# Optimization experiments

Measured on AMD Instinct MI355X. Metric: run time of the kernel, lower is better.

Reference implementation:

```python
import jax, jax.numpy as jnp
import numpy as np

B, C, F, T = 4, 128, 64, 2048
QK_OUT = 4      # conv out channels for q/k
ATT_DIM = 10    # hard-coded linear out dim


def setup_inputs() -> dict:
    key = jax.random.key(0)
    ks = jax.random.split(key, 12)
    s = 0.05
    x = jax.random.normal(ks[0], (B, C, F, T), dtype=jnp.float32)
    Wq_conv = jax.random.normal(ks[1], (QK_OUT, C), dtype=jnp.float32) * s
    bq_conv = jax.random.normal(ks[2], (QK_OUT,), dtype=jnp.float32) * s
    Wq_lin = jax.random.normal(ks[3], (ATT_DIM, QK_OUT * F), dtype=jnp.float32) * s
    bq_lin = jax.random.normal(ks[4], (ATT_DIM,), dtype=jnp.float32) * s
    Wk_conv = jax.random.normal(ks[5], (QK_OUT, C), dtype=jnp.float32) * s
    bk_conv = jax.random.normal(ks[6], (QK_OUT,), dtype=jnp.float32) * s
    Wk_lin = jax.random.normal(ks[7], (ATT_DIM, QK_OUT * F), dtype=jnp.float32) * s
    bk_lin = jax.random.normal(ks[8], (ATT_DIM,), dtype=jnp.float32) * s
    Wv_conv = jax.random.normal(ks[9], (C, C), dtype=jnp.float32) * s
    bv_conv = jax.random.normal(ks[10], (C,), dtype=jnp.float32) * s
    return {
        "x": x,
        "Wq_conv": Wq_conv, "bq_conv": bq_conv,
        "Wq_lin": Wq_lin, "bq_lin": bq_lin,
        "Wk_conv": Wk_conv, "bk_conv": bk_conv,
        "Wk_lin": Wk_lin, "bk_lin": bk_lin,
        "Wv_conv": Wv_conv, "bv_conv": bv_conv,
    }


def reference(x, Wq_conv, bq_conv, Wq_lin, bq_lin,
              Wk_conv, bk_conv, Wk_lin, bk_lin, Wv_conv, bv_conv):
    b, c, f, t = x.shape
    # 1x1 conv == per-pixel channel matmul
    q = jnp.einsum('bcft,oc->boft', x, Wq_conv) + bq_conv[None, :, None, None]
    q = q.reshape(b, QK_OUT * f, t).transpose(0, 2, 1)          # [b, t, 4f]
    q = q @ Wq_lin.T + bq_lin                                    # [b, t, 10]
    k = jnp.einsum('bcft,oc->boft', x, Wk_conv) + bk_conv[None, :, None, None]
    k = k.reshape(b, QK_OUT * f, t).transpose(0, 2, 1)
    k = k @ Wk_lin.T + bk_lin                                    # [b, t, 10]
    energy = jnp.einsum('bid,bjd->bij', q, k)                    # [b, t, t]
    attention = jax.nn.softmax(energy, axis=-1)
    v = jnp.einsum('bcft,oc->boft', x, Wv_conv) + bv_conv[None, :, None, None]
    v = v.reshape(b, c * f, t)                                   # [b, cf, t]
    # out = value @ attention^T : out[n, i] = sum_j v[n, j] * attention[i, j]
    out = jnp.einsum('bnj,bij->bni', v, attention)
    return out.reshape(b, c, f, t)
```

## Files before the change

### kernel.cpp

```cpp
#include <hip/hip_runtime.h>
#include <hip/hip_bf16.h>

#define Bq 4
#define Cc 128
#define Ff 64
#define Tt 2048
#define CF 8192
#define NCHUNK 32
#define CHUNK 256

typedef __attribute__((ext_vector_type(4))) float f32x4;
typedef __attribute__((ext_vector_type(8))) short bf16x8;

__device__ inline ushort f2bf(float f) {
    __hip_bfloat16 h = __float2bfloat16(f);
    return *reinterpret_cast<ushort*>(&h);
}

__device__ inline void gload_lds16(const void* g, void* l) {
    __builtin_amdgcn_global_load_lds(
        (const __attribute__((address_space(1))) void*)g,
        (__attribute__((address_space(3))) void*)l, 16, 0, 0);
}

__global__ void k_prep(const float* __restrict__ Wq_lin, const float* __restrict__ Wq_conv,
                       const float* __restrict__ Wk_lin, const float* __restrict__ Wk_conv,
                       const float* __restrict__ bq_conv, const float* __restrict__ bq_lin,
                       const float* __restrict__ bk_conv, const float* __restrict__ bk_lin,
                       const float* __restrict__ Wv,
                       float* __restrict__ weff, float* __restrict__ cqk,
                       ushort* __restrict__ Wvb) {
    int blk = blockIdx.x;
    if (blk < 640) {
        int gid = blk * 256 + threadIdx.x;
        if (gid >= CF * 20) return;
        int cf = gid / 20, d = gid % 20;
        int c = cf >> 6, f = cf & 63;
        float s = 0.f;
        if (d < 10) {
            #pragma unroll
            for (int o = 0; o < 4; ++o) s += Wq_lin[d * 256 + o * 64 + f] * Wq_conv[o * 128 + c];
        } else {
            int dd = d - 10;
            #pragma unroll
            for (int o = 0; o < 4; ++o) s += Wk_lin[dd * 256 + o * 64 + f] * Wk_conv[o * 128 + c];
        }
        weff[cf * 20 + d] = s;
    } else if (blk < 704) {
        int i = (blk - 640) * 256 + threadIdx.x;
        if (i < 16384) Wvb[i] = f2bf(Wv[i]);
    } else {
        int d = threadIdx.x;
        if (d >= 20) return;
        float s;
        if (d < 10) {
            s = bq_lin[d];
            for (int o = 0; o < 4; ++o) {
                float bb = bq_conv[o];
                for (int f = 0; f < 64; ++f) s += Wq_lin[d * 256 + o * 64 + f] * bb;
            }
        } else {
            int dd = d - 10;
            s = bk_lin[dd];
            for (int o = 0; o < 4; ++o) {
                float bb = bk_conv[o];
                for (int f = 0; f < 64; ++f) s += Wk_lin[dd * 256 + o * 64 + f] * bb;
            }
        }
        cqk[d] = s;
    }
}

__global__ __launch_bounds__(256) void k_qk(const float* __restrict__ x,
                                            const float* __restrict__ weff,
                                            float* __restrict__ partial,
                                            ushort* __restrict__ xbf) {
    int blk = blockIdx.x;
    int tt = blk & 3;
    int ch = (blk >> 2) & 31;
    int b  = blk >> 7;
    int t = tt * 512 + threadIdx.x * 2;
    const float* xb = x + (size_t)b * CF * Tt;
    ushort* xob = xbf + (size_t)b * CF * Tt;
    float acc[20][2];
    #pragma unroll
    for (int d = 0; d < 20; ++d) { acc[d][0] = 0.f; acc[d][1] = 0.f; }
    int cf0 = ch * CHUNK;
    for (int cf = cf0; cf < cf0 + CHUNK; ++cf) {
        float2 xv = *(const float2*)(xb + (size_t)cf * Tt + t);
        *(ushort2*)(xob + (size_t)cf * Tt + t) = make_ushort2(f2bf(xv.x), f2bf(xv.y));
        const float* w = weff + cf * 20;
        #pragma unroll
        for (int d = 0; d < 20; ++d) {
            float wv = w[d];
            acc[d][0] += wv * xv.x;
            acc[d][1] += wv * xv.y;
        }
    }
    float* pb = partial + (size_t)(b * NCHUNK + ch) * 20 * Tt;
    #pragma unroll
    for (int d = 0; d < 20; ++d)
        *(float2*)(pb + (size_t)d * Tt + t) = make_float2(acc[d][0], acc[d][1]);
}

__global__ void k_qkred(const float* __restrict__ partial, const float* __restrict__ cqk,
                        float* __restrict__ Q, float* __restrict__ Kt) {
    int t = blockIdx.x * 256 + threadIdx.x;
    int d = blockIdx.y;
    int b = t >> 11, tl = t & 2047;
    float s = cqk[d];
    #pragma unroll 4
    for (int ch = 0; ch < NCHUNK; ++ch)
        s += partial[((size_t)(b * NCHUNK + ch) * 20 + d) * Tt + tl];
    if (d < 10) Q[(size_t)(b * 2048 + tl) * 10 + d] = s;
    else        Kt[((size_t)b * 10 + (d - 10)) * Tt + tl] = s;
}

__global__ __launch_bounds__(256) void k_att(const float* __restrict__ Q,
                                             const float* __restrict__ Kt,
                                             ushort* __restrict__ A) {
    int bi = blockIdx.x;
    int b = bi >> 11;
    __shared__ float qs[10];
    __shared__ float wmax[4];
    __shared__ float wsum[4];
    int tid = threadIdx.x;
    int lane = tid & 63, wid = tid >> 6;
    if (tid < 10) qs[tid] = Q[(size_t)bi * 10 + tid];
    __syncthreads();
    float q[10];
    #pragma unroll
    for (int d = 0; d < 10; ++d) q[d] = qs[d];
    const float* kb = Kt + (size_t)b * 10 * Tt;
    float e[8];
    #pragma unroll
    for (int v = 0; v < 8; ++v) e[v] = 0.f;
    #pragma unroll
    for (int d = 0; d < 10; ++d) {
        float qd = q[d];
        const float* kd = kb + (size_t)d * Tt + tid * 2;
        #pragma unroll
        for (int g = 0; g < 4; ++g) {
            float2 kv = *(const float2*)(kd + g * 512);
            e[2 * g]     += qd * kv.x;
            e[2 * g + 1] += qd * kv.y;
        }
    }
    float m = e[0];
    #pragma unroll
    for (int v = 1; v < 8; ++v) m = fmaxf(m, e[v]);
    #pragma unroll
    for (int off = 32; off > 0; off >>= 1) m = fmaxf(m, __shfl_xor(m, off));
    if (lane == 0) wmax[wid] = m;
    __syncthreads();
    float M = fmaxf(fmaxf(wmax[0], wmax[1]), fmaxf(wmax[2], wmax[3]));
    float sum = 0.f;
    #pragma unroll
    for (int v = 0; v < 8; ++v) { e[v] = __expf(e[v] - M); sum += e[v]; }
    #pragma unroll
    for (int off = 32; off > 0; off >>= 1) sum += __shfl_xor(sum, off);
    if (lane == 0) wsum[wid] = sum;
    __syncthreads();
    float inv = 1.f / (wsum[0] + wsum[1] + wsum[2] + wsum[3]);
    ushort* arow = A + (size_t)bi * Tt + tid * 2;
    #pragma unroll
    for (int g = 0; g < 4; ++g)
        *(ushort2*)(arow + g * 512) =
            make_ushort2(f2bf(e[2 * g] * inv), f2bf(e[2 * g + 1] * inv));
}

__global__ __launch_bounds__(512, 2) void k_pv_conv(const ushort* __restrict__ Xb,
                                                    const ushort* __restrict__ Ab,
                                                    const ushort* __restrict__ Wvb,
                                                    const float* __restrict__ bv,
                                                    float* __restrict__ out) {
    __shared__ float smemf[32768];
    char* smem = (char*)smemf;
    int fb = blockIdx.x, ib = blockIdx.y, b = blockIdx.z;
    int f0 = fb * 2;
    int tid = threadIdx.x;
    int w = tid >> 6, l = tid & 63;
    int wm = w >> 2, wn = w & 3;
    int frow = l & 15, q = l >> 4, f7 = frow & 7;

    const ushort* xb0 = Xb + (size_t)b * CF * Tt + (size_t)f0 * Tt;
    const ushort* ab0 = Ab + (size_t)b * Tt * Tt + (size_t)ib * 256 * Tt;

    int row_l = w * 8 + (l >> 3);
    int col_s = (((l & 7) ^ (l >> 3)) << 3);
    const ushort* srcB[4]; const ushort* srcA[4];
    #pragma unroll
    for (int g = 0; g < 4; ++g) {
        int row = g * 64 + row_l;
        srcB[g] = ab0 + (size_t)row * Tt + col_s;
        int n = (row & 127) * 64 + (row >> 7);
        srcA[g] = xb0 + (size_t)n * Tt + col_s;
    }

#define STG_B(g) gload_lds16(srcB[g] + k1, nb + (g) * 8192 + w * 1024)
#define STG_A(g) gload_lds16(srcA[g] + k1, nb + 32768 + (g) * 8192 + w * 1024)

    int swzk0 = (q ^ f7) << 4;
    int swzk1 = ((4 + q) ^ f7) << 4;
    int aBase = 32768 + (wm * 128 + frow) * 128;
    int bBase = (wn * 64 + frow) * 128;

#define READ_A(cb, MH)                                                          \
    _Pragma("unroll")                                                           \
    for (int mm = 0; mm < 4; ++mm) {                                            \
        afr[mm][0] = *(const bf16x8*)((cb) + aBase + (MH) * 8192 + mm * 2048 + swzk0); \
        afr[mm][1] = *(const bf16x8*)((cb) + aBase + (MH) * 8192 + mm * 2048 + swzk1); \
    }
#define READ_B(cb, NH, DST)                                                     \
    _Pragma("unroll")                                                           \
    for (int nn = 0; nn < 2; ++nn) {                                            \
        DST[nn][0] = *(const bf16x8*)((cb) + bBase + (NH) * 4096 + nn * 2048 + swzk0); \
        DST[nn][1] = *(const bf16x8*)((cb) + bBase + (NH) * 4096 + nn * 2048 + swzk1); \
    }
#define MFMA_Q(MH, NH, BFR)                                                     \
    __builtin_amdgcn_s_setprio(1);                                              \
    _Pragma("unroll")                                                           \
    for (int kk = 0; kk < 2; ++kk)                                              \
        _Pragma("unroll")                                                       \
        for (int mm = 0; mm < 4; ++mm)                                          \
            _Pragma("unroll")                                                   \
            for (int nn = 0; nn < 2; ++nn)                                      \
                acc[(MH) * 4 + mm][(NH) * 2 + nn] =                             \
                    __builtin_amdgcn_mfma_f32_16x16x32_bf16(                    \
                        afr[mm][kk], BFR[nn][kk],                               \
                        acc[(MH) * 4 + mm][(NH) * 2 + nn], 0, 0, 0);            \
    __builtin_amdgcn_s_setprio(0);

#define BARX() __builtin_amdgcn_s_barrier()
#define LGKM0() asm volatile("s_waitcnt lgkmcnt(0)" ::: "memory")

#define ITER_BODY(CBUF, NBUF, T, ST) do {                                \
        const char* cb = (CBUF);                                         \
        char* nb = (NBUF);                                               \
        int k1 = ((T) + 1) * 64;                                         \
        if (!(ST)) asm volatile("s_waitcnt vmcnt(0)" ::: "memory");      \
        bf16x8 afr[4][2], bfr0[2][2], bfr1[2][2];                        \
                                                 \
        READ_A(cb, 0)                                                    \
        READ_B(cb, 0, bfr0)                                              \
        if (ST) { STG_B(0); STG_B(1); }                                  \
        BARX(); LGKM0();                                                 \
        MFMA_Q(0, 0, bfr0)                                               \
        BARX();                                                          \
                                                 \
        READ_B(cb, 1, bfr1)                                              \
        if (ST) { STG_B(2); STG_B(3); }                                  \
        BARX(); LGKM0();                                                 \
        MFMA_Q(0, 1, bfr1)                                               \
        asm volatile("s_waitcnt vmcnt(4)" ::: "memory");                 \
        BARX();         \
                                                 \
        READ_A(cb, 1)                                                    \
        if (ST) { STG_A(0); STG_A(2); }                                  \
        BARX(); LGKM0();                                                 \
        MFMA_Q(1, 1, bfr1)                                               \
        BARX();                                                          \
                      \
        if (ST) { STG_A(1); STG_A(3); }                                  \
        MFMA_Q(1, 0, bfr0)                                               \
        asm volatile("s_waitcnt vmcnt(2)" ::: "memory");                 \
        BARX();                 \
    } while (0)

    f32x4 acc[8][4];
    #pragma unroll
    for (int m = 0; m < 8; ++m)
        #pragma unroll
        for (int n = 0; n < 4; ++n) acc[m][n] = (f32x4){0.f, 0.f, 0.f, 0.f};

    {
        char* nb = smem;
        int k1 = 0;
        STG_B(0); STG_B(1); STG_B(2); STG_B(3);
        STG_A(0); STG_A(2); STG_A(1); STG_A(3);
    }
    asm volatile("s_waitcnt vmcnt(2)" ::: "memory");
    __builtin_amdgcn_s_barrier();

    #pragma unroll 1
    for (int tp = 0; tp < 15; ++tp) {
        ITER_BODY(smem,         smem + 65536, 2 * tp,     true);
        ITER_BODY(smem + 65536, smem,         2 * tp + 1, true);
    }
    ITER_BODY(smem,         smem + 65536, 30, true);
    ITER_BODY(smem + 65536, smem,         31, false);
    __syncthreads();

    {
        char* Yt = smem + wm * 65536;
        #pragma unroll
        for (int n = 0; n < 4; ++n) {
            int i = wn * 64 + n * 16 + frow;
            int swzy = (i & 7) << 4;
            #pragma unroll
            for (int m = 0; m < 8; ++m) {
                int cp = m * 16 + q * 4;
                ushort4 v;
                v.x = f2bf(acc[m][n][0]); v.y = f2bf(acc[m][n][1]);
                v.z = f2bf(acc[m][n][2]); v.w = f2bf(acc[m][n][3]);
                *(ushort4*)(Yt + ((i * 256 + cp * 2) ^ swzy)) = v;
            }
        }
    }
    __syncthreads();

    int fh = w >> 2, wn2 = w & 3;
    const char* ytb = smem + fh * 65536;
    f32x4 acc2[8][4];
    #pragma unroll
    for (int m = 0; m < 8; ++m)
        #pragma unroll
        for (int n = 0; n < 4; ++n) acc2[m][n] = (f32x4){0.f, 0.f, 0.f, 0.f};
    #pragma unroll
    for (int ks = 0; ks < 4; ++ks) {
        int kofs = ks * 32 + q * 8;
        bf16x8 a2[8], b2[4];
        #pragma unroll
        for (int m = 0; m < 8; ++m)
            a2[m] = *(const bf16x8*)&Wvb[(m * 16 + frow) * 128 + kofs];
        #pragma unroll
        for (int n = 0; n < 4; ++n) {
            int i = wn2 * 64 + n * 16 + frow;
            b2[n] = *(const bf16x8*)(ytb + ((i * 256 + kofs * 2) ^ ((i & 7) << 4)));
        }
        #pragma unroll
        for (int m = 0; m < 8; ++m)
            #pragma unroll
            for (int n = 0; n < 4; ++n)
                acc2[m][n] = __builtin_amdgcn_mfma_f32_16x16x32_bf16(a2[m], b2[n], acc2[m][n], 0, 0, 0);
    }

    float* ob = out + (size_t)b * CF * Tt + (size_t)(f0 + fh) * Tt
                    + (size_t)ib * 256 + wn2 * 64;
    #pragma unroll
    for (int m = 0; m < 8; ++m) {
        #pragma unroll
        for (int r = 0; r < 4; ++r) {
            int c = m * 16 + q * 4 + r;
            float bvv = bv[c];
            #pragma unroll
            for (int n = 0; n < 4; ++n)
                ob[(size_t)c * 64 * Tt + n * 16 + frow] = acc2[m][n][r] + bvv;
        }
    }
#undef STG_A
#undef STG_B
#undef READ_A
#undef READ_B
#undef MFMA_Q
#undef ITER_BODY
#undef BARX
#undef LGKM0
}

extern "C" void kernel_launch(void* const* d_in, const int* in_sizes, int n_in,
                              void* d_out, int out_size, void* d_ws, size_t ws_size,
                              hipStream_t stream) {
    const float* x       = (const float*)d_in[0];
    const float* Wq_conv = (const float*)d_in[1];
    const float* bq_conv = (const float*)d_in[2];
    const float* Wq_lin  = (const float*)d_in[3];
    const float* bq_lin  = (const float*)d_in[4];
    const float* Wk_conv = (const float*)d_in[5];
    const float* bk_conv = (const float*)d_in[6];
    const float* Wk_lin  = (const float*)d_in[7];
    const float* bk_lin  = (const float*)d_in[8];
    const float* Wv      = (const float*)d_in[9];
    const float* bv      = (const float*)d_in[10];
    float* out = (float*)d_out;

    float* ws   = (float*)d_ws;
    float* weff = ws;
    float* cqk  = weff + 163840;
    float* part = cqk + 32;
    float* Qb   = part + 5242880;
    float* Ktb  = Qb + 81920;
    float* Abf_f = Ktb + 81920;
    float* Xbf_f = Abf_f + 8388608;
    float* Wvb_f = Xbf_f + 33554432;
    ushort* Abf = (ushort*)Abf_f;
    ushort* Xbf = (ushort*)Xbf_f;
    ushort* Wvb = (ushort*)Wvb_f;

    k_prep <<<705, 256, 0, stream>>>(Wq_lin, Wq_conv, Wk_lin, Wk_conv,
                                     bq_conv, bq_lin, bk_conv, bk_lin, Wv,
                                     weff, cqk, Wvb);
    k_qk   <<<512, 256, 0, stream>>>(x, weff, part, Xbf);
    k_qkred<<<dim3(32, 20), 256, 0, stream>>>(part, cqk, Qb, Ktb);
    k_att  <<<8192, 256, 0, stream>>>(Qb, Ktb, Abf);
    k_pv_conv<<<dim3(32, 8, 4), 512, 0, stream>>>(Xbf, Abf, Wvb, bv, out);
}
```

Measured before the change: 445.0 us.

## Halve PV kernel workgroup to 4 waves with larger per-wave tiles

Restructures the fused PV+conv kernel from 8 waves of 512 threads to 4 waves of 256 threads. Each wave now computes a 128x128 output tile with 64 accumulators, which raises MFMA reuse of the LDS fragments. Each thread issues twice as many global-to-LDS loads, and the vmcnt waits are adjusted to match. The second GEMM is split into two passes to limit register pressure. The cost is much higher VGPR use and fewer waves available to hide latency.

```diff
diff --git a/kernel.cpp b/kernel.cpp
--- a/kernel.cpp
+++ b/kernel.cpp
@@ -169,7 +169,7 @@
             make_ushort2(f2bf(e[2 * g] * inv), f2bf(e[2 * g + 1] * inv));
 }
 
-__global__ __launch_bounds__(512, 2) void k_pv_conv(const ushort* __restrict__ Xb,
+__global__ __launch_bounds__(256, 1) void k_pv_conv(const ushort* __restrict__ Xb,
                                                     const ushort* __restrict__ Ab,
                                                     const ushort* __restrict__ Wvb,
                                                     const float* __restrict__ bv,
@@ -180,7 +180,7 @@
     int f0 = fb * 2;
     int tid = threadIdx.x;
     int w = tid >> 6, l = tid & 63;
-    int wm = w >> 2, wn = w & 3;
+    int wm = w >> 1, wn = w & 1;
     int frow = l & 15, q = l >> 4, f7 = frow & 7;
 
     const ushort* xb0 = Xb + (size_t)b * CF * Tt + (size_t)f0 * Tt;
@@ -191,19 +191,21 @@
     const ushort* srcB[4]; const ushort* srcA[4];
     #pragma unroll
     for (int g = 0; g < 4; ++g) {
-        int row = g * 64 + row_l;
-        srcB[g] = ab0 + (size_t)row * Tt + col_s;
-        int n = (row & 127) * 64 + (row >> 7);
-        srcA[g] = xb0 + (size_t)n * Tt + col_s;
-    }
-
-#define STG_B(g) gload_lds16(srcB[g] + k1, nb + (g) * 8192 + w * 1024)
-#define STG_A(g) gload_lds16(srcA[g] + k1, nb + 32768 + (g) * 8192 + w * 1024)
+        srcB[g] = ab0 + (size_t)(g * 64 + row_l) * Tt + col_s;
+        srcA[g] = xb0 + (size_t)(((g & 1) * 64 + row_l) * 64 + (g >> 1)) * Tt + col_s;
+    }
+    const size_t HOFFB = (size_t)32 * Tt;
+    const size_t HOFFA = (size_t)2048 * Tt;
+
+#define STG_B(g, h) gload_lds16(srcB[g] + k1 + (h) * HOFFB, \
+                                nb + (g) * 8192 + (h) * 4096 + w * 1024)
+#define STG_A(g, h) gload_lds16(srcA[g] + k1 + (h) * HOFFA, \
+                                nb + 32768 + (g) * 8192 + (h) * 4096 + w * 1024)
 
     int swzk0 = (q ^ f7) << 4;
     int swzk1 = ((4 + q) ^ f7) << 4;
     int aBase = 32768 + (wm * 128 + frow) * 128;
-    int bBase = (wn * 64 + frow) * 128;
+    int bBase = (wn * 128 + frow) * 128;
 
 #define READ_A(cb, MH)                                                          \
     _Pragma("unroll")                                                           \
@@ -213,9 +215,9 @@
     }
 #define READ_B(cb, NH, DST)                                                     \
     _Pragma("unroll")                                                           \
-    for (int nn = 0; nn < 2; ++nn) {                                            \
-        DST[nn][0] = *(const bf16x8*)((cb) + bBase + (NH) * 4096 + nn * 2048 + swzk0); \
-        DST[nn][1] = *(const bf16x8*)((cb) + bBase + (NH) * 4096 + nn * 2048 + swzk1); \
+    for (int nn = 0; nn < 4; ++nn) {                                            \
+        DST[nn][0] = *(const bf16x8*)((cb) + bBase + (NH) * 8192 + nn * 2048 + swzk0); \
+        DST[nn][1] = *(const bf16x8*)((cb) + bBase + (NH) * 8192 + nn * 2048 + swzk1); \
     }
 #define MFMA_Q(MH, NH, BFR)                                                     \
     __builtin_amdgcn_s_setprio(1);                                              \
@@ -224,11 +226,11 @@
         _Pragma("unroll")                                                       \
         for (int mm = 0; mm < 4; ++mm)                                          \
             _Pragma("unroll")                                                   \
-            for (int nn = 0; nn < 2; ++nn)                                      \
-                acc[(MH) * 4 + mm][(NH) * 2 + nn] =                             \
+            for (int nn = 0; nn < 4; ++nn)                                      \
+                acc[(MH) * 4 + mm][(NH) * 4 + nn] =                             \
                     __builtin_amdgcn_mfma_f32_16x16x32_bf16(                    \
                         afr[mm][kk], BFR[nn][kk],                               \
-                        acc[(MH) * 4 + mm][(NH) * 2 + nn], 0, 0, 0);            \
+                        acc[(MH) * 4 + mm][(NH) * 4 + nn], 0, 0, 0);            \
     __builtin_amdgcn_s_setprio(0);
 
 #define BARX() __builtin_amdgcn_s_barrier()
@@ -237,49 +239,51 @@
 #define ITER_BODY(CBUF, NBUF, T, ST) do {                                \
         const char* cb = (CBUF);                                         \
         char* nb = (NBUF);                                               \
-        int k1 = ((T) + 1) * 64;                                         \
+        size_t k1 = (size_t)((T) + 1) * 64;                              \
         if (!(ST)) asm volatile("s_waitcnt vmcnt(0)" ::: "memory");      \
-        bf16x8 afr[4][2], bfr0[2][2], bfr1[2][2];                        \
-                                                 \
+        bf16x8 afr[4][2], bfr0[4][2], bfr1[4][2];                        \
+                                             \
         READ_A(cb, 0)                                                    \
         READ_B(cb, 0, bfr0)                                              \
-        if (ST) { STG_B(0); STG_B(1); }                                  \
+        if (ST) { STG_B(0,0); STG_B(0,1); STG_B(2,0); STG_B(2,1); }      \
         BARX(); LGKM0();                                                 \
         MFMA_Q(0, 0, bfr0)                                               \
         BARX();                                                          \
-                                                 \
+                                             \
         READ_B(cb, 1, bfr1)                                              \
-        if (ST) { STG_B(2); STG_B(3); }                                  \
+        if (ST) { STG_B(1,0); STG_B(1,1); STG_B(3,0); STG_B(3,1); }      \
         BARX(); LGKM0();                                                 \
         MFMA_Q(0, 1, bfr1)                                               \
-        asm volatile("s_waitcnt vmcnt(4)" ::: "memory");                 \
-        BARX();         \
-                                                 \
+        asm volatile("s_waitcnt vmcnt(8)" ::: "memory");                 \
+        BARX();        \
+                                             \
         READ_A(cb, 1)                                                    \
-        if (ST) { STG_A(0); STG_A(2); }                                  \
+        if (ST) { STG_A(0,0); STG_A(0,1); STG_A(2,0); STG_A(2,1); }      \
         BARX(); LGKM0();                                                 \
         MFMA_Q(1, 1, bfr1)                                               \
         BARX();                                                          \
-                      \
-        if (ST) { STG_A(1); STG_A(3); }                                  \
+                           \
+        if (ST) { STG_A(1,0); STG_A(1,1); STG_A(3,0); STG_A(3,1); }      \
         MFMA_Q(1, 0, bfr0)                                               \
-        asm volatile("s_waitcnt vmcnt(2)" ::: "memory");                 \
-        BARX();                 \
+        asm volatile("s_waitcnt vmcnt(4)" ::: "memory");                 \
+        BARX();        \
     } while (0)
 
-    f32x4 acc[8][4];
+    f32x4 acc[8][8];
     #pragma unroll
     for (int m = 0; m < 8; ++m)
         #pragma unroll
-        for (int n = 0; n < 4; ++n) acc[m][n] = (f32x4){0.f, 0.f, 0.f, 0.f};
+        for (int n = 0; n < 8; ++n) acc[m][n] = (f32x4){0.f, 0.f, 0.f, 0.f};
 
     {
         char* nb = smem;
-        int k1 = 0;
-        STG_B(0); STG_B(1); STG_B(2); STG_B(3);
-        STG_A(0); STG_A(2); STG_A(1); STG_A(3);
-    }
-    asm volatile("s_waitcnt vmcnt(2)" ::: "memory");
+        size_t k1 = 0;
+        STG_B(0,0); STG_B(0,1); STG_B(2,0); STG_B(2,1);
+        STG_B(1,0); STG_B(1,1); STG_B(3,0); STG_B(3,1);
+        STG_A(0,0); STG_A(0,1); STG_A(2,0); STG_A(2,1);
+        STG_A(1,0); STG_A(1,1); STG_A(3,0); STG_A(3,1);
+    }
+    asm volatile("s_waitcnt vmcnt(4)" ::: "memory");
     __builtin_amdgcn_s_barrier();
 
     #pragma unroll 1
@@ -294,8 +298,8 @@
     {
         char* Yt = smem + wm * 65536;
         #pragma unroll
-        for (int n = 0; n < 4; ++n) {
-            int i = wn * 64 + n * 16 + frow;
+        for (int n = 0; n < 8; ++n) {
+            int i = wn * 128 + n * 16 + frow;
             int swzy = (i & 7) << 4;
             #pragma unroll
             for (int m = 0; m < 8; ++m) {
@@ -309,43 +313,45 @@
     }
     __syncthreads();
 
-    int fh = w >> 2, wn2 = w & 3;
+    int fh = w >> 1, wn2 = w & 1;
     const char* ytb = smem + fh * 65536;
-    f32x4 acc2[8][4];
-    #pragma unroll
-    for (int m = 0; m < 8; ++m)
-        #pragma unroll
-        for (int n = 0; n < 4; ++n) acc2[m][n] = (f32x4){0.f, 0.f, 0.f, 0.f};
-    #pragma unroll
-    for (int ks = 0; ks < 4; ++ks) {
-        int kofs = ks * 32 + q * 8;
-        bf16x8 a2[8], b2[4];
+    #pragma unroll 1
+    for (int p = 0; p < 2; ++p) {
+        f32x4 acc2[8][4];
         #pragma unroll
         for (int m = 0; m < 8; ++m)
-            a2[m] = *(const bf16x8*)&Wvb[(m * 16 + frow) * 128 + kofs];
-        #pragma unroll
-        for (int n = 0; n < 4; ++n) {
-            int i = wn2 * 64 + n * 16 + frow;
-            b2[n] = *(const bf16x8*)(ytb + ((i * 256 + kofs * 2) ^ ((i & 7) << 4)));
-        }
-        #pragma unroll
-        for (int m = 0; m < 8; ++m)
-            #pragma unroll
-            for (int n = 0; n < 4; ++n)
-                acc2[m][n] = __builtin_amdgcn_mfma_f32_16x16x32_bf16(a2[m], b2[n], acc2[m][n], 0, 0, 0);
-    }
-
-    float* ob = out + (size_t)b * CF * Tt + (size_t)(f0 + fh) * Tt
-                    + (size_t)ib * 256 + wn2 * 64;
-    #pragma unroll
-    for (int m = 0; m < 8; ++m) {
-        #pragma unroll
-        for (int r = 0; r < 4; ++r) {
-            int c = m * 16 + q * 4 + r;
-            float bvv = bv[c];
-            #pragma unroll
-            for (int n = 0; n < 4; ++n)
-                ob[(size_t)c * 64 * Tt + n * 16 + frow] = acc2[m][n][r] + bvv;
+            #pragma unroll
+            for (int n = 0; n < 4; ++n) acc2[m][n] = (f32x4){0.f, 0.f, 0.f, 0.f};
+        #pragma unroll
+        for (int ks = 0; ks < 4; ++ks) {
+            int kofs = ks * 32 + q * 8;
+            bf16x8 a2[8], b2[4];
+            #pragma unroll
+            for (int m = 0; m < 8; ++m)
+                a2[m] = *(const bf16x8*)&Wvb[(m * 16 + frow) * 128 + kofs];
+            #pragma unroll
+            for (int n = 0; n < 4; ++n) {
+                int i = wn2 * 128 + p * 64 + n * 16 + frow;
+                b2[n] = *(const bf16x8*)(ytb + ((i * 256 + kofs * 2) ^ ((i & 7) << 4)));
+            }
+            #pragma unroll
+            for (int m = 0; m < 8; ++m)
+                #pragma unroll
+                for (int n = 0; n < 4; ++n)
+                    acc2[m][n] = __builtin_amdgcn_mfma_f32_16x16x32_bf16(a2[m], b2[n], acc2[m][n], 0, 0, 0);
+        }
+        float* ob = out + (size_t)b * CF * Tt + (size_t)(f0 + fh) * Tt
+                        + (size_t)ib * 256 + wn2 * 128 + p * 64;
+        #pragma unroll
+        for (int m = 0; m < 8; ++m) {
+            #pragma unroll
+            for (int r = 0; r < 4; ++r) {
+                int c = m * 16 + q * 4 + r;
+                float bvv = bv[c];
+                #pragma unroll
+                for (int n = 0; n < 4; ++n)
+                    ob[(size_t)c * 64 * Tt + n * 16 + frow] = acc2[m][n][r] + bvv;
+            }
         }
     }
 #undef STG_A
@@ -393,5 +399,5 @@
     k_qk   <<<512, 256, 0, stream>>>(x, weff, part, Xbf);
     k_qkred<<<dim3(32, 20), 256, 0, stream>>>(part, cqk, Qb, Ktb);
     k_att  <<<8192, 256, 0, stream>>>(Qb, Ktb, Abf);
-    k_pv_conv<<<dim3(32, 8, 4), 512, 0, stream>>>(Xbf, Abf, Wvb, bv, out);
-}
+    k_pv_conv<<<dim3(32, 8, 4), 256, 0, stream>>>(Xbf, Abf, Wvb, bv, out);
+}
```

Result: slower. 494.9 us (+11.2%).

## Shrink PV GEMM tile to 256x128 with BK=32 and 4 waves per block

Applied to the files above, without the earlier changes.

Restructures the fused attention-value GEMM plus value-conv kernel. Blocks go from 512 threads with a 256x256 output tile and K-step 64 to 256 threads with a 256x128 tile and K-step 32, using a new LDS swizzle and a simpler one-barrier-per-stage pipeline. LDS use drops from 128KB to 48KB, which allows more resident blocks and twice as many blocks in the grid. The value-conv epilogue is serialized over the two f rows through a shared Y buffer. In exchange, each tile gets less reuse, the X operand is reloaded across twice as many i-blocks, and there are more barriers per unit of K.

```diff
diff --git a/kernel.cpp b/kernel.cpp
--- a/kernel.cpp
+++ b/kernel.cpp
@@ -169,102 +169,75 @@
             make_ushort2(f2bf(e[2 * g] * inv), f2bf(e[2 * g + 1] * inv));
 }
 
-__global__ __launch_bounds__(512, 2) void k_pv_conv(const ushort* __restrict__ Xb,
+__global__ __launch_bounds__(256, 2) void k_pv_conv(const ushort* __restrict__ Xb,
                                                     const ushort* __restrict__ Ab,
                                                     const ushort* __restrict__ Wvb,
                                                     const float* __restrict__ bv,
                                                     float* __restrict__ out) {
-    __shared__ float smemf[32768];
+    __shared__ float smemf[12288];
     char* smem = (char*)smemf;
     int fb = blockIdx.x, ib = blockIdx.y, b = blockIdx.z;
     int f0 = fb * 2;
     int tid = threadIdx.x;
     int w = tid >> 6, l = tid & 63;
-    int wm = w >> 2, wn = w & 3;
-    int frow = l & 15, q = l >> 4, f7 = frow & 7;
+    int wm = w >> 1, wn = w & 1;
+    int frow = l & 15, q = l >> 4;
 
     const ushort* xb0 = Xb + (size_t)b * CF * Tt + (size_t)f0 * Tt;
-    const ushort* ab0 = Ab + (size_t)b * Tt * Tt + (size_t)ib * 256 * Tt;
-
-    int row_l = w * 8 + (l >> 3);
-    int col_s = (((l & 7) ^ (l >> 3)) << 3);
-    const ushort* srcB[4]; const ushort* srcA[4];
+    const ushort* ab0 = Ab + (size_t)b * Tt * Tt + (size_t)ib * 128 * Tt;
+
+    int row_l = w * 16 + (l >> 2);
+    int col_s = (((l & 3) ^ ((l >> 3) & 3)) << 3);
+    const ushort* srcA[4]; const ushort* srcB[2];
     #pragma unroll
     for (int g = 0; g < 4; ++g) {
-        int row = g * 64 + row_l;
-        srcB[g] = ab0 + (size_t)row * Tt + col_s;
-        int n = (row & 127) * 64 + (row >> 7);
-        srcA[g] = xb0 + (size_t)n * Tt + col_s;
-    }
-
-#define STG_B(g) gload_lds16(srcB[g] + k1, nb + (g) * 8192 + w * 1024)
-#define STG_A(g) gload_lds16(srcA[g] + k1, nb + 32768 + (g) * 8192 + w * 1024)
-
-    int swzk0 = (q ^ f7) << 4;
-    int swzk1 = ((4 + q) ^ f7) << 4;
-    int aBase = 32768 + (wm * 128 + frow) * 128;
-    int bBase = (wn * 64 + frow) * 128;
-
-#define READ_A(cb, MH)                                                          \
-    _Pragma("unroll")                                                           \
-    for (int mm = 0; mm < 4; ++mm) {                                            \
-        afr[mm][0] = *(const bf16x8*)((cb) + aBase + (MH) * 8192 + mm * 2048 + swzk0); \
-        afr[mm][1] = *(const bf16x8*)((cb) + aBase + (MH) * 8192 + mm * 2048 + swzk1); \
-    }
-#define READ_B(cb, NH, DST)                                                     \
-    _Pragma("unroll")                                                           \
-    for (int nn = 0; nn < 2; ++nn) {                                            \
-        DST[nn][0] = *(const bf16x8*)((cb) + bBase + (NH) * 4096 + nn * 2048 + swzk0); \
-        DST[nn][1] = *(const bf16x8*)((cb) + bBase + (NH) * 4096 + nn * 2048 + swzk1); \
-    }
-#define MFMA_Q(MH, NH, BFR)                                                     \
-    __builtin_amdgcn_s_setprio(1);                                              \
-    _Pragma("unroll")                                                           \
-    for (int kk = 0; kk < 2; ++kk)                                              \
-        _Pragma("unroll")                                                       \
-        for (int mm = 0; mm < 4; ++mm)                                          \
-            _Pragma("unroll")                                                   \
-            for (int nn = 0; nn < 2; ++nn)                                      \
-                acc[(MH) * 4 + mm][(NH) * 2 + nn] =                             \
-                    __builtin_amdgcn_mfma_f32_16x16x32_bf16(                    \
-                        afr[mm][kk], BFR[nn][kk],                               \
-                        acc[(MH) * 4 + mm][(NH) * 2 + nn], 0, 0, 0);            \
-    __builtin_amdgcn_s_setprio(0);
-
-#define BARX() __builtin_amdgcn_s_barrier()
-#define LGKM0() asm volatile("s_waitcnt lgkmcnt(0)" ::: "memory")
+        int arow = g * 64 + row_l;
+        srcA[g] = xb0 + (size_t)((arow & 127) * 64 + (arow >> 7)) * Tt + col_s;
+    }
+    #pragma unroll
+    for (int h = 0; h < 2; ++h)
+        srcB[h] = ab0 + (size_t)(h * 64 + row_l) * Tt + col_s;
+
+#define STG_A(g) gload_lds16(srcA[g] + k1, nb + (g) * 4096 + w * 1024)
+#define STG_B(h) gload_lds16(srcB[h] + k1, nb + 16384 + (h) * 4096 + w * 1024)
+
+    int swz = (q ^ ((frow >> 1) & 3)) << 4;
+    int aBase = (wm * 128 + frow) * 64 + swz;
+    int bBase = 16384 + (wn * 64 + frow) * 64 + swz;
+
+#define READ_A(cb)                                                       \
+    _Pragma("unroll")                                                    \
+    for (int mm = 0; mm < 8; ++mm)                                       \
+        afr[mm] = *(const bf16x8*)((cb) + aBase + mm * 1024);
+#define READ_B(cb)                                                       \
+    _Pragma("unroll")                                                    \
+    for (int nn = 0; nn < 4; ++nn)                                       \
+        bfr[nn] = *(const bf16x8*)((cb) + bBase + nn * 1024);
 
 #define ITER_BODY(CBUF, NBUF, T, ST) do {                                \
         const char* cb = (CBUF);                                         \
         char* nb = (NBUF);                                               \
-        int k1 = ((T) + 1) * 64;                                         \
-        if (!(ST)) asm volatile("s_waitcnt vmcnt(0)" ::: "memory");      \
-        bf16x8 afr[4][2], bfr0[2][2], bfr1[2][2];                        \
-                                                 \
-        READ_A(cb, 0)                                                    \
-        READ_B(cb, 0, bfr0)                                              \
+        int k1 = ((T) + 1) * 32;                                         \
+        bf16x8 afr[8], bfr[4];                                           \
+                              \
+        READ_A(cb)                                                       \
+        if (ST) { STG_A(0); STG_A(1); STG_A(2); STG_A(3); }              \
+        if (ST) asm volatile("s_waitcnt vmcnt(4)" ::: "memory");         \
+        else    asm volatile("s_waitcnt vmcnt(0)" ::: "memory");         \
+        __builtin_amdgcn_s_barrier();       \
+                               \
+        READ_B(cb)                                                       \
         if (ST) { STG_B(0); STG_B(1); }                                  \
-        BARX(); LGKM0();                                                 \
-        MFMA_Q(0, 0, bfr0)                                               \
-        BARX();                                                          \
-                                                 \
-        READ_B(cb, 1, bfr1)                                              \
-        if (ST) { STG_B(2); STG_B(3); }                                  \
-        BARX(); LGKM0();                                                 \
-        MFMA_Q(0, 1, bfr1)                                               \
-        asm volatile("s_waitcnt vmcnt(4)" ::: "memory");                 \
-        BARX();         \
-                                                 \
-        READ_A(cb, 1)                                                    \
-        if (ST) { STG_A(0); STG_A(2); }                                  \
-        BARX(); LGKM0();                                                 \
-        MFMA_Q(1, 1, bfr1)                                               \
-        BARX();                                                          \
-                      \
-        if (ST) { STG_A(1); STG_A(3); }                                  \
-        MFMA_Q(1, 0, bfr0)                                               \
-        asm volatile("s_waitcnt vmcnt(2)" ::: "memory");                 \
-        BARX();                 \
+        __builtin_amdgcn_s_setprio(1);                                   \
+        _Pragma("unroll")                                                \
+        for (int mm = 0; mm < 8; ++mm)                                   \
+            _Pragma("unroll")                                            \
+            for (int nn = 0; nn < 4; ++nn)                               \
+                acc[mm][nn] = __builtin_amdgcn_mfma_f32_16x16x32_bf16(   \
+                    afr[mm], bfr[nn], acc[mm][nn], 0, 0, 0);             \
+        __builtin_amdgcn_s_setprio(0);                                   \
+        if (ST) asm volatile("s_waitcnt vmcnt(2)" ::: "memory");         \
+        __builtin_amdgcn_s_barrier();       \
     } while (0)
 
     f32x4 acc[8][4];
@@ -276,86 +249,84 @@
     {
         char* nb = smem;
         int k1 = 0;
-        STG_B(0); STG_B(1); STG_B(2); STG_B(3);
-        STG_A(0); STG_A(2); STG_A(1); STG_A(3);
+        STG_A(0); STG_A(1); STG_A(2); STG_A(3);
+        STG_B(0); STG_B(1);
     }
     asm volatile("s_waitcnt vmcnt(2)" ::: "memory");
     __builtin_amdgcn_s_barrier();
 
     #pragma unroll 1
-    for (int tp = 0; tp < 15; ++tp) {
-        ITER_BODY(smem,         smem + 65536, 2 * tp,     true);
-        ITER_BODY(smem + 65536, smem,         2 * tp + 1, true);
-    }
-    ITER_BODY(smem,         smem + 65536, 30, true);
-    ITER_BODY(smem + 65536, smem,         31, false);
+    for (int tp = 0; tp < 31; ++tp) {
+        ITER_BODY(smem,         smem + 24576, 2 * tp,     true);
+        ITER_BODY(smem + 24576, smem,         2 * tp + 1, true);
+    }
+    ITER_BODY(smem,         smem + 24576, 62, true);
+    ITER_BODY(smem + 24576, smem,         63, false);
     __syncthreads();
 
-    {
-        char* Yt = smem + wm * 65536;
-        #pragma unroll
-        for (int n = 0; n < 4; ++n) {
-            int i = wn * 64 + n * 16 + frow;
-            int swzy = (i & 7) << 4;
+    char* Yt = smem;
+    #pragma unroll 1
+    for (int fh = 0; fh < 2; ++fh) {
+        if (wm == fh) {
+            #pragma unroll
+            for (int n = 0; n < 4; ++n) {
+                int i = wn * 64 + n * 16 + frow;
+                int swzy = (i & 7) << 4;
+                #pragma unroll
+                for (int m = 0; m < 8; ++m) {
+                    int cp = m * 16 + q * 4;
+                    ushort4 v;
+                    v.x = f2bf(acc[m][n][0]); v.y = f2bf(acc[m][n][1]);
+                    v.z = f2bf(acc[m][n][2]); v.w = f2bf(acc[m][n][3]);
+                    *(ushort4*)(Yt + ((i * 256 + cp * 2) ^ swzy)) = v;
+                }
+            }
+        }
+        __syncthreads();
+        f32x4 acc2[8][2];
+        #pragma unroll
+        for (int m = 0; m < 8; ++m) {
+            acc2[m][0] = (f32x4){0.f, 0.f, 0.f, 0.f};
+            acc2[m][1] = (f32x4){0.f, 0.f, 0.f, 0.f};
+        }
+        #pragma unroll
+        for (int ks = 0; ks < 4; ++ks) {
+            int kofs = ks * 32 + q * 8;
+            bf16x8 a2[8], b2[2];
+            #pragma unroll
+            for (int m = 0; m < 8; ++m)
+                a2[m] = *(const bf16x8*)&Wvb[(m * 16 + frow) * 128 + kofs];
+            #pragma unroll
+            for (int n = 0; n < 2; ++n) {
+                int i = w * 32 + n * 16 + frow;
+                b2[n] = *(const bf16x8*)(Yt + ((i * 256 + kofs * 2) ^ ((i & 7) << 4)));
+            }
             #pragma unroll
             for (int m = 0; m < 8; ++m) {
-                int cp = m * 16 + q * 4;
-                ushort4 v;
-                v.x = f2bf(acc[m][n][0]); v.y = f2bf(acc[m][n][1]);
-                v.z = f2bf(acc[m][n][2]); v.w = f2bf(acc[m][n][3]);
-                *(ushort4*)(Yt + ((i * 256 + cp * 2) ^ swzy)) = v;
-            }
-        }
-    }
-    __syncthreads();
-
-    int fh = w >> 2, wn2 = w & 3;
-    const char* ytb = smem + fh * 65536;
-    f32x4 acc2[8][4];
-    #pragma unroll
-    for (int m = 0; m < 8; ++m)
-        #pragma unroll
-        for (int n = 0; n < 4; ++n) acc2[m][n] = (f32x4){0.f, 0.f, 0.f, 0.f};
-    #pragma unroll
-    for (int ks = 0; ks < 4; ++ks) {
-        int kofs = ks * 32 + q * 8;
-        bf16x8 a2[8], b2[4];
-        #pragma unroll
-        for (int m = 0; m < 8; ++m)
-            a2[m] = *(const bf16x8*)&Wvb[(m * 16 + frow) * 128 + kofs];
-        #pragma unroll
-        for (int n = 0; n < 4; ++n) {
-            int i = wn2 * 64 + n * 16 + frow;
-            b2[n] = *(const bf16x8*)(ytb + ((i * 256 + kofs * 2) ^ ((i & 7) << 4)));
-        }
-        #pragma unroll
-        for (int m = 0; m < 8; ++m)
-            #pragma unroll
-            for (int n = 0; n < 4; ++n)
-                acc2[m][n] = __builtin_amdgcn_mfma_f32_16x16x32_bf16(a2[m], b2[n], acc2[m][n], 0, 0, 0);
-    }
-
-    float* ob = out + (size_t)b * CF * Tt + (size_t)(f0 + fh) * Tt
-                    + (size_t)ib * 256 + wn2 * 64;
-    #pragma unroll
-    for (int m = 0; m < 8; ++m) {
-        #pragma unroll
-        for (int r = 0; r < 4; ++r) {
-            int c = m * 16 + q * 4 + r;
-            float bvv = bv[c];
-            #pragma unroll
-            for (int n = 0; n < 4; ++n)
-                ob[(size_t)c * 64 * Tt + n * 16 + frow] = acc2[m][n][r] + bvv;
-        }
+                acc2[m][0] = __builtin_amdgcn_mfma_f32_16x16x32_bf16(a2[m], b2[0], acc2[m][0], 0, 0, 0);
+                acc2[m][1] = __builtin_amdgcn_mfma_f32_16x16x32_bf16(a2[m], b2[1], acc2[m][1], 0, 0, 0);
+            }
+        }
+        float* ob = out + (size_t)b * CF * Tt + (size_t)(f0 + fh) * Tt
+                        + (size_t)ib * 128;
+        #pragma unroll
+        for (int m = 0; m < 8; ++m) {
+            #pragma unroll
+            for (int r = 0; r < 4; ++r) {
+                int c = m * 16 + q * 4 + r;
+                float bvv = bv[c];
+                #pragma unroll
+                for (int n = 0; n < 2; ++n)
+                    ob[(size_t)c * 64 * Tt + w * 32 + n * 16 + frow] = acc2[m][n][r] + bvv;
+            }
+        }
+        __syncthreads();
     }
 #undef STG_A
 #undef STG_B
 #undef READ_A
 #undef READ_B
-#undef MFMA_Q
 #undef ITER_BODY
-#undef BARX
-#undef LGKM0
 }
 
 extern "C" void kernel_launch(void* const* d_in, const int* in_sizes, int n_in,
@@ -393,5 +364,5 @@
     k_qk   <<<512, 256, 0, stream>>>(x, weff, part, Xbf);
     k_qkred<<<dim3(32, 20), 256, 0, stream>>>(part, cqk, Qb, Ktb);
     k_att  <<<8192, 256, 0, stream>>>(Qb, Ktb, Abf);
-    k_pv_conv<<<dim3(32, 8, 4), 512, 0, stream>>>(Xbf, Abf, Wvb, bv, out);
-}
+    k_pv_conv<<<dim3(32, 16, 4), 256, 0, stream>>>(Xbf, Abf, Wvb, bv, out);
+}
```

New measurement: 668.1 us. +50.1%, slower.
